# Kernel optimization log

Measured on AMD Instinct MI355X. Metric: run time of the kernel, lower is better.

## Reference

```python
import jax, jax.numpy as jnp
import numpy as np
from jax import lax

# FPN anchor layout: 800x800 image, 3 anchors/loc, strides 4,8,16,32,64
LEVEL_ANCHORS = [120000, 30000, 7500, 1875, 507]
PRE_NMS_TOP_N = 1000   # per level (test mode)
POST_NMS_TOP_N = 1000
NMS_THRESH = 0.7
MIN_SIZE = 1e-3


def setup_inputs() -> dict:
    key = jax.random.key(0)
    k1, k2, k3, k4 = jax.random.split(key, 4)
    A = sum(LEVEL_ANCHORS)
    bs = 2
    predicts = jax.random.normal(k1, (bs, A, 4), jnp.float32) * 0.1
    objectness = jax.random.normal(k2, (bs, A, 1), jnp.float32)
    cxy = jax.random.uniform(k3, (A, 2), jnp.float32, 0.0, 800.0)
    wh = jax.random.uniform(k4, (A, 2), jnp.float32, 16.0, 128.0)
    anchors = jnp.concatenate([cxy - 0.5 * wh, cxy + 0.5 * wh], axis=-1)
    valid_size = jnp.full((bs, 2), 800.0, jnp.float32)  # (w, h) per image
    return {"predicts": predicts, "objectness": objectness,
            "anchors": anchors, "valid_size": valid_size}


def _decode(predicts, anchors):
    # BoxCoder.decoder with weights [1,1,1,1]
    awh = anchors[:, 2:] - anchors[:, :2]          # [A,2]
    axy = anchors[:, :2] + 0.5 * awh               # [A,2]
    xy = axy + predicts[..., :2] * awh             # [bs,A,2] center
    wh = jnp.exp(predicts[..., 2:]) * awh          # [bs,A,2]
    x1y1 = xy - 0.5 * wh
    return jnp.concatenate([x1y1, x1y1 + wh], axis=-1)  # [bs,A,4]


def _per_level_topk_idx(scores):
    # scores: [bs, A] -> concat of per-level top-k indices (global anchor ids)
    idx_list, offset = [], 0
    for n in LEVEL_ANCHORS:
        k = min(PRE_NMS_TOP_N, n)
        _, top = lax.top_k(scores[:, offset:offset + n], k)
        idx_list.append(top + offset)
        offset += n
    return jnp.concatenate(idx_list, axis=1)  # [bs, K]


def _nms_keep(boxes, valid, thresh):
    # boxes sorted by score desc; returns boolean keep mask (sequential NMS)
    x1, y1, x2, y2 = boxes[:, 0], boxes[:, 1], boxes[:, 2], boxes[:, 3]
    area = (x2 - x1) * (y2 - y1)
    xx1 = jnp.maximum(x1[:, None], x1[None, :])
    yy1 = jnp.maximum(y1[:, None], y1[None, :])
    xx2 = jnp.minimum(x2[:, None], x2[None, :])
    yy2 = jnp.minimum(y2[:, None], y2[None, :])
    inter = jnp.maximum(xx2 - xx1, 0.0) * jnp.maximum(yy2 - yy1, 0.0)
    iou = inter / (area[:, None] + area[None, :] - inter + 1e-9)
    sup = iou > thresh                                   # [N,N]
    N = boxes.shape[0]
    ar = jnp.arange(N)

    def body(i, keep):
        suppressed = jnp.any((ar < i) & keep & sup[i])
        return keep.at[i].set(keep[i] & ~suppressed)

    return lax.fori_loop(0, N, body, valid)


def _filter_image(boxes, scores, lvls, wh):
    # boxes [K,4], scores [K], lvls [K] int, wh [2]=(w,h)
    w, h = wh[0], wh[1]
    x1 = jnp.clip(boxes[:, 0], 0.0, w)
    y1 = jnp.clip(boxes[:, 1], 0.0, h)
    x2 = jnp.clip(boxes[:, 2], 0.0, w)
    y2 = jnp.clip(boxes[:, 3], 0.0, h)
    boxes = jnp.stack([x1, y1, x2, y2], axis=-1)
    valid = (x2 - x1 > MIN_SIZE) & (y2 - y1 > MIN_SIZE)
    s = jnp.where(valid, scores, -jnp.inf)
    order = jnp.argsort(-s)
    boxes, s, lvls, valid = boxes[order], s[order], lvls[order], valid[order]
    # batched_nms: offset each level into a disjoint coordinate range
    max_coord = lax.stop_gradient(jnp.max(boxes)) + 1.0
    off = lvls.astype(boxes.dtype) * max_coord
    keep = _nms_keep(lax.stop_gradient(boxes) + off[:, None], valid, NMS_THRESH)
    # take first POST_NMS_TOP_N kept (boxes are score-sorted)
    rank = jnp.cumsum(keep) - 1
    slot = jnp.where(keep & (rank < POST_NMS_TOP_N), rank, POST_NMS_TOP_N)
    out_b = jnp.zeros((POST_NMS_TOP_N + 1, 4), boxes.dtype).at[slot].set(boxes)[:POST_NMS_TOP_N]
    out_s = jnp.zeros((POST_NMS_TOP_N + 1,), s.dtype).at[slot].set(
        jnp.where(keep, s, 0.0))[:POST_NMS_TOP_N]
    return out_b, out_s


def reference(predicts, objectness, anchors, valid_size):
    bs = predicts.shape[0]
    proposals = _decode(predicts, anchors)            # [bs,A,4]
    scores = objectness[..., 0]                       # [bs,A]
    idx = _per_level_topk_idx(scores)                 # [bs,K]
    bidx = jnp.arange(bs)[:, None]
    boxes = proposals[bidx, idx]                      # [bs,K,4]
    sc = scores[bidx, idx]                            # [bs,K]
    levels_all = jnp.concatenate(
        [jnp.full((n,), i, jnp.int32) for i, n in enumerate(LEVEL_ANCHORS)])
    lvl = levels_all[idx]                             # [bs,K]
    final_boxes, final_scores = jax.vmap(_filter_image)(boxes, sc, lvl, valid_size)
    return final_boxes, final_scores
```

## Files before the change

kernel.cpp:

```cpp
#include <hip/hip_runtime.h>

typedef unsigned int u32;
typedef unsigned long long u64;

#define A_TOT    159882
#define BS       2
#define KTOP     1000
#define CAND_CAP 4096
#define HB       4096
#define ABLK     4096
#define NBH      40
#define EPT      16

static const size_t HIST12_OFF   = 0;
static const size_t CUT_OFF      = 131072;
static const size_t CCNT_OFF     = 131104;
static const size_t MAXC_OFF     = 131136;
static const size_t NV_OFF       = 131144;
static const size_t CHUNKANY_OFF = 131200;
static const size_t ZERO_END     = 132480;
static const size_t CAND_OFF     = 132480;
static const size_t LKEY2_OFF    = 394624;
static const size_t LBOX_OFF     = 476544;
static const size_t LSC_OFF      = 640384;
static const size_t RANK_OFF     = 681344;
static const size_t MASK_OFF     = 759168;

__device__ __forceinline__ int level_of(int a) {
  if (a < 120000) return 0;
  if (a < 150000) return 1;
  if (a < 157500) return 2;
  if (a < 159375) return 3;
  return 4;
}

__device__ __forceinline__ u32 dkey(float s) {
  u32 b = __float_as_uint(s);
  return (b & 0x80000000u) ? b : (~b & 0x7FFFFFFFu);
}

__device__ __forceinline__ void decode_clip(const float* __restrict__ pred,
                                            const float* __restrict__ anch,
                                            const float* __restrict__ vs,
                                            int b, int a,
                                            float& x1c, float& y1c, float& x2c, float& y2c,
                                            bool& valid) {
  const float* pp = pred + ((size_t)b * A_TOT + (size_t)a) * 4;
  const float* aa = anch + (size_t)a * 4;
  float ax1 = aa[0], ay1 = aa[1], ax2 = aa[2], ay2 = aa[3];
  float px = pp[0], py = pp[1], pw = pp[2], ph = pp[3];
  float aw  = __fsub_rn(ax2, ax1);
  float ah  = __fsub_rn(ay2, ay1);
  float acx = __fadd_rn(ax1, __fmul_rn(0.5f, aw));
  float acy = __fadd_rn(ay1, __fmul_rn(0.5f, ah));
  float cx  = __fadd_rn(acx, __fmul_rn(px, aw));
  float cy  = __fadd_rn(acy, __fmul_rn(py, ah));
  float w   = __fmul_rn(expf(pw), aw);
  float h   = __fmul_rn(expf(ph), ah);
  float x1  = __fsub_rn(cx, __fmul_rn(0.5f, w));
  float y1  = __fsub_rn(cy, __fmul_rn(0.5f, h));
  float x2  = __fadd_rn(x1, w);
  float y2  = __fadd_rn(y1, h);
  float Wv = vs[b * 2 + 0], Hv = vs[b * 2 + 1];
  x1c = fminf(fmaxf(x1, 0.0f), Wv);
  y1c = fminf(fmaxf(y1, 0.0f), Hv);
  x2c = fminf(fmaxf(x2, 0.0f), Wv);
  y2c = fminf(fmaxf(y2, 0.0f), Hv);
  valid = (__fsub_rn(x2c, x1c) > 0.001f) && (__fsub_rn(y2c, y1c) > 0.001f);
}

__device__ __forceinline__ void bitonic_u64(u64* arr, int N, int t, int nt) {
  for (int k = 2; k <= N; k <<= 1) {
    for (int j = k >> 1; j > 0; j >>= 1) {
      __syncthreads();
      for (int i = t; i < N; i += nt) {
        int ixj = i ^ j;
        if (ixj > i) {
          u64 x = arr[i], y = arr[ixj];
          bool up = ((i & k) == 0);
          if (up ? (x > y) : (x < y)) { arr[i] = y; arr[ixj] = x; }
        }
      }
    }
  }
  __syncthreads();
}

__device__ __forceinline__ u64 shfl_xor_u64(u64 x, int lanemask) {
  u32 lo = (u32)x, hi = (u32)(x >> 32);
  lo = (u32)__shfl_xor((int)lo, lanemask);
  hi = (u32)__shfl_xor((int)hi, lanemask);
  return ((u64)hi << 32) | (u64)lo;
}

__device__ __forceinline__ void regsort2048(u64 v[8], int tid, u64* arr) {
  for (int k = 2; k <= 2048; k <<= 1) {
    for (int j = k >> 1; j > 0; j >>= 1) {
      if (j >= 512) {
        __syncthreads();
#pragma unroll
        for (int e = 0; e < 8; ++e) arr[tid * 8 + e] = v[e];
        __syncthreads();
#pragma unroll
        for (int e = 0; e < 8; ++e) {
          int i = tid * 8 + e, p = i ^ j;
          u64 o = arr[p];
          bool up = ((i & k) == 0);
          bool keepmin = ((i < p) == up);
          v[e] = keepmin ? (v[e] < o ? v[e] : o) : (v[e] > o ? v[e] : o);
        }
      } else if (j >= 8) {
        int dl = j >> 3;
#pragma unroll
        for (int e = 0; e < 8; ++e) {
          int i = tid * 8 + e;
          u64 o = shfl_xor_u64(v[e], dl);
          bool up = ((i & k) == 0);
          bool keepmin = (((tid & dl) == 0) == up);
          v[e] = keepmin ? (v[e] < o ? v[e] : o) : (v[e] > o ? v[e] : o);
        }
      } else {
#pragma unroll
        for (int e = 0; e < 8; ++e) {
          int pe = e ^ j;
          if (pe > e) {
            int i = tid * 8 + e;
            bool up = ((i & k) == 0);
            u64 a = v[e], b2 = v[pe];
            bool sw = up ? (a > b2) : (a < b2);
            if (sw) { v[e] = b2; v[pe] = a; }
          }
        }
      }
    }
  }
  __syncthreads();
#pragma unroll
  for (int e = 0; e < 8; ++e) arr[tid * 8 + e] = v[e];
  __syncthreads();
}

__global__ void k_zero(char* __restrict__ ws) {
  size_t i = (size_t)blockIdx.x * blockDim.x + threadIdx.x;
  if (i * 4 < ZERO_END) ((u32*)ws)[i] = 0u;
}

__global__ void k_hist12(const float* __restrict__ obj, char* __restrict__ ws) {
  __shared__ u32 h[2 * HB];
  int tid = threadIdx.x;
  int b = blockIdx.x / NBH, loc = blockIdx.x % NBH;
  int start = loc * ABLK;
  int l0 = level_of(start);
  if (l0 >= 4) return;
  for (int i = tid; i < 2 * HB; i += 256) h[i] = 0u;
  __syncthreads();
  for (int it = 0; it < EPT; ++it) {
    int a = start + it * 256 + tid;
    if (a < A_TOT) {
      int l = level_of(a);
      if (l < 4) {
        u32 d = dkey(obj[(size_t)b * A_TOT + a]);
        atomicAdd(&h[(u32)(l - l0) * HB + (d >> 20)], 1u);
      }
    }
  }
  __syncthreads();
  int lend = level_of(min(start + ABLK - 1, A_TOT - 1));
  int nseg = ((l0 + 1 <= lend) && (l0 + 1 < 4)) ? 2 : 1;
  for (int s = 0; s < nseg; ++s) {
    u32* gh = (u32*)(ws + HIST12_OFF) + (size_t)(b * 4 + l0 + s) * HB;
    for (int i = tid; i < HB; i += 256) {
      u32 v = h[s * HB + i];
      if (v) atomicAdd(&gh[i], v);
    }
  }
}

__global__ void k_compactsel(const float* __restrict__ obj, char* __restrict__ ws) {
  __shared__ u32 scan[256];
  __shared__ u32 cutv[2];
  __shared__ u32 lcnt[2], gbase[2];
  int tid = threadIdx.x, lane = tid & 63;
  int b = blockIdx.x / NBH, loc = blockIdx.x % NBH;
  int start = loc * ABLK;
  int l0 = level_of(start);
  if (l0 >= 4) return;
  int lend = level_of(min(start + ABLK - 1, A_TOT - 1));
  int nseg = ((l0 + 1 <= lend) && (l0 + 1 < 4)) ? 2 : 1;
  if (tid < 2) lcnt[tid] = 0;
  for (int s = 0; s < nseg; ++s) {
    int seg = b * 4 + l0 + s;
    const u32* gh = (const u32*)(ws + HIST12_OFF) + (size_t)seg * HB;
    u32 vals[16]; u32 acc = 0;
    for (int q = 0; q < 16; ++q) { vals[q] = gh[tid * 16 + q]; acc += vals[q]; }
    __syncthreads();
    scan[tid] = acc; __syncthreads();
    for (int d = 1; d < 256; d <<= 1) {
      u32 x = (tid >= d) ? scan[tid - d] : 0u; __syncthreads();
      scan[tid] += x; __syncthreads();
    }
    u32 incl = scan[tid], prev = incl - acc;
    if (prev < KTOP && incl >= KTOP) {
      u32 run = prev; int cb = HB - 1;
      for (int q = 0; q < 16; ++q) { run += vals[q]; if (run >= KTOP) { cb = tid * 16 + q; break; } }
      cutv[s] = (u32)cb;
      ((u32*)(ws + CUT_OFF))[seg] = (u32)cb;
    }
  }
  __syncthreads();
  u32 dv[EPT], slotv[EPT], passm = 0, sim = 0;
  for (int it = 0; it < EPT; ++it) {
    int a = start + it * 256 + tid;
    bool pass = false; u32 si = 0, d = 0;
    if (a < A_TOT) {
      int l = level_of(a);
      if (l < 4) {
        si = (u32)(l - l0);
        d = dkey(obj[(size_t)b * A_TOT + a]);
        pass = (d >> 20) <= cutv[si];
      }
    }
    dv[it] = d;
    u64 mp = __ballot(pass);
    u64 m1 = __ballot(pass && si == 1);
    u64 m0 = mp & ~m1;
    u32 slot = 0;
    if (m0) {
      int ld = __builtin_ctzll(m0);
      u32 wb = 0;
      if (lane == ld) wb = atomicAdd(&lcnt[0], (u32)__popcll(m0));
      wb = __shfl(wb, ld);
      if (pass && si == 0) slot = wb + (u32)__popcll(m0 & ((1ull << lane) - 1ull));
    }
    if (m1) {
      int ld = __builtin_ctzll(m1);
      u32 wb = 0;
      if (lane == ld) wb = atomicAdd(&lcnt[1], (u32)__popcll(m1));
      wb = __shfl(wb, ld);
      if (pass && si == 1) slot = wb + (u32)__popcll(m1 & ((1ull << lane) - 1ull));
    }
    slotv[it] = slot;
    if (pass) { passm |= 1u << it; if (si) sim |= 1u << it; }
  }
  __syncthreads();
  if (tid < 2)
    gbase[tid] = lcnt[tid] ? atomicAdd((u32*)(ws + CCNT_OFF) + (b * 4 + l0 + tid), lcnt[tid]) : 0u;
  __syncthreads();
  for (int it = 0; it < EPT; ++it) {
    if ((passm >> it) & 1u) {
      int a = start + it * 256 + tid;
      u32 si = (sim >> it) & 1u;
      int seg = b * 4 + l0 + (int)si;
      u32 gslot = gbase[si] + slotv[it];
      if (gslot < CAND_CAP)
        ((u64*)(ws + CAND_OFF))[(size_t)seg * CAND_CAP + gslot] =
            ((u64)dv[it] << 32) | (u32)a;
    }
  }
}

__global__ void k_sortdec(const float* __restrict__ pred, const float* __restrict__ obj,
                          const float* __restrict__ anch, const float* __restrict__ vs,
                          char* __restrict__ ws) {
  __shared__ u64 arr[CAND_CAP];
  __shared__ float4 dboxL[1024];
  __shared__ float dscL[1024];
  __shared__ u64 vmask[16];
  int tid = threadIdx.x, lane = tid & 63, wv = tid >> 6;
  int P = blockIdx.x, b = P / 5, l = P % 5;
  int n;
  if (l == 4) {
    n = 507;
    u64 v[8];
#pragma unroll
    for (int e = 0; e < 8; ++e) {
      int idx = tid * 8 + e;
      if (idx < 507) {
        int a = 159375 + idx;
        v[e] = ((u64)dkey(obj[(size_t)b * A_TOT + a]) << 32) | (u32)a;
      } else v[e] = ~0ull;
    }
    regsort2048(v, tid, arr);
  } else {
    n = KTOP;
    int seg = b * 4 + l;
    u32 cnt = min(((const u32*)(ws + CCNT_OFF))[seg], (u32)CAND_CAP);
    const u64* cand = (const u64*)(ws + CAND_OFF) + (size_t)seg * CAND_CAP;
    if (cnt <= 2048) {
      u64 v[8];
#pragma unroll
      for (int e = 0; e < 8; ++e) {
        int idx = tid * 8 + e;
        v[e] = (idx < (int)cnt) ? cand[idx] : ~0ull;
      }
      regsort2048(v, tid, arr);
    } else {
      for (int i = tid; i < CAND_CAP; i += 256) arr[i] = (i < (int)cnt) ? cand[i] : ~0ull;
      int N = 2048; while (N < (int)cnt) N <<= 1;
      bitonic_u64(arr, N, tid, 256);
    }
  }
  float m = 0.0f;
  for (int k = 0; k < 4; ++k) {
    int j = k * 256 + tid;
    bool vb = false;
    if (j < n) {
      u64 key = arr[j];
      int a = (int)(u32)key;
      float x1, y1, x2, y2; bool valid;
      decode_clip(pred, anch, vs, b, a, x1, y1, x2, y2, valid);
      m = fmaxf(m, fmaxf(fmaxf(x1, y1), fmaxf(x2, y2)));
      dboxL[j] = make_float4(x1, y1, x2, y2);
      dscL[j] = obj[(size_t)b * A_TOT + a];
      vb = valid;
    }
    u64 bal = __ballot(vb);
    if (lane == 0) vmask[k * 4 + wv] = bal;
  }
  for (int off = 32; off; off >>= 1) m = fmaxf(m, __shfl_xor(m, off));
  if (lane == 0) atomicMax((u32*)(ws + MAXC_OFF) + b, __float_as_uint(m));
  __syncthreads();
  if (tid < 64) {
    int base = 0;
    for (int j0 = 0; j0 < n; j0 += 64) {
      int j = j0 + lane;
      bool v = (j < n) && ((vmask[j0 >> 6] >> lane) & 1ull);
      u64 mm = __ballot(v);
      int r = base + __popcll(mm & ((1ull << lane) - 1ull));
      if (v) {
        ((u64*)(ws + LKEY2_OFF))[(size_t)P * 1024 + r] = arr[j];
        ((float4*)(ws + LBOX_OFF))[(size_t)P * 1024 + r] = dboxL[j];
        ((float*)(ws + LSC_OFF))[(size_t)P * 1024 + r] = dscL[j];
      }
      base += __popcll(mm);
    }
    if (lane == 0) ((u32*)(ws + NV_OFF))[P] = (u32)base;
  }
}

__device__ __forceinline__ int lbound(const u64* __restrict__ arr, int n, u64 key) {
  int lo = 0, hi = n;
  while (lo < hi) { int mid = (lo + hi) >> 1; if (arr[mid] < key) lo = mid + 1; else hi = mid; }
  return lo;
}

__global__ void k_maskrank(char* __restrict__ ws) {
  int tid = threadIdx.x, bid = blockIdx.x;
  if (bid < 10) {
    int P = bid, b = P / 5, l = P % 5;
    int nv = (int)((const u32*)(ws + NV_OFF))[P];
    const u64* lkey = (const u64*)(ws + LKEY2_OFF);
    const u32* nvp = (const u32*)(ws + NV_OFF);
    for (int i = tid; i < nv; i += 256) {
      u64 key = lkey[(size_t)P * 1024 + i];
      int r = i;
      for (int l2 = 0; l2 < 5; ++l2) {
        if (l2 == l) continue;
        int P2 = b * 5 + l2;
        r += lbound(lkey + (size_t)P2 * 1024, (int)nvp[P2], key);
      }
      ((u32*)(ws + RANK_OFF))[(size_t)P * 1024 + i] = (u32)r;
    }
  }
  int idx = bid * 256 + tid;
  int w = idx & 15;
  int i = (idx >> 4) & 1023;
  int P = idx >> 14;
  if (P >= 10) return;
  int b = P / 5, l = P % 5;
  int n = (int)((const u32*)(ws + NV_OFF))[P];
  int W = (n + 63) >> 6;
  if (i >= n || w >= W) return;
  float M = __uint_as_float(((const u32*)(ws + MAXC_OFF))[b]);
  float maxc = __fadd_rn(M, 1.0f);
  float off = __fmul_rn((float)l, maxc);
  const float4* lbox = (const float4*)(ws + LBOX_OFF) + (size_t)P * 1024;
  float4 bi = lbox[i];
  bi.x = __fadd_rn(bi.x, off); bi.y = __fadd_rn(bi.y, off);
  bi.z = __fadd_rn(bi.z, off); bi.w = __fadd_rn(bi.w, off);
  float ai = __fmul_rn(__fsub_rn(bi.z, bi.x), __fsub_rn(bi.w, bi.y));
  u64 word = 0;
  int j0 = w << 6;
  int jn = min(64, n - j0);
  for (int jj = 0; jj < jn; ++jj) {
    float4 bj = lbox[j0 + jj];
    bj.x = __fadd_rn(bj.x, off); bj.y = __fadd_rn(bj.y, off);
    bj.z = __fadd_rn(bj.z, off); bj.w = __fadd_rn(bj.w, off);
    float xx1 = fmaxf(bi.x, bj.x);
    float yy1 = fmaxf(bi.y, bj.y);
    float xx2 = fminf(bi.z, bj.z);
    float yy2 = fminf(bi.w, bj.w);
    float iw = fmaxf(__fsub_rn(xx2, xx1), 0.0f);
    float ih = fmaxf(__fsub_rn(yy2, yy1), 0.0f);
    float inter = __fmul_rn(iw, ih);
    float aj = __fmul_rn(__fsub_rn(bj.z, bj.x), __fsub_rn(bj.w, bj.y));
    float den = __fadd_rn(__fsub_rn(__fadd_rn(ai, aj), inter), 1e-9f);
    float iou = __fdiv_rn(inter, den);
    if (iou > 0.7f) word |= (1ull << jj);
  }
  if (i >= j0 && i < j0 + 64) word &= ~(1ull << (i - j0));
  ((u64*)(ws + MASK_OFF))[(size_t)P * 16000 + (size_t)i * W + w] = word;
  if (word)
    atomicOr((u64*)(ws + CHUNKANY_OFF) + (size_t)P * 16 + (i >> 6), 1ull << (i & 63));
}

__global__ __launch_bounds__(320)
void k_scanfin(float* __restrict__ out, char* __restrict__ ws) {
  __shared__ u64 keeps[5][16];
  __shared__ u64 kb[80];
  __shared__ u32 sb[128];
  __shared__ u32 pfx[80];
  __shared__ u32 nvs[5];
  int tid = threadIdx.x, w = tid >> 6, lane = tid & 63;
  int b = blockIdx.x;
  for (int i = tid; i < 80; i += 320) kb[i] = 0ull;
  for (int i = tid; i < 4000; i += 320) out[(size_t)b * 4000 + i] = 0.0f;
  for (int i = tid; i < 1000; i += 320) out[8000 + (size_t)b * 1000 + i] = 0.0f;
  if (tid < 5) nvs[tid] = ((const u32*)(ws + NV_OFF))[b * 5 + tid];

  int P = b * 5 + w;
  int n = (int)((const u32*)(ws + NV_OFF))[P];
  int W = (n + 63) >> 6;
  const u64* maskg = (const u64*)(ws + MASK_OFF) + (size_t)P * 16000;
  u64 ca = (lane < 16) ? ((const u64*)(ws + CHUNKANY_OFF))[(size_t)P * 16 + lane] : 0ull;
  u64 dpre[16];
#pragma unroll
  for (int c = 0; c < 16; ++c) {
    int row = (c << 6) + lane;
    dpre[c] = (c < W && row < n) ? maskg[(size_t)row * W + c] : 0ull;
  }
  u64 removed = 0ull, keepw = 0ull;
#pragma unroll
  for (int c = 0; c < 16; ++c) {
    if (c >= W) break;
    int rb = c << 6;
    int rows = min(64, n - rb);
    u64 rowsmask = (rows == 64) ? ~0ull : ((1ull << rows) - 1ull);
    u64 curw = __shfl(removed, c);
    u64 cand = ~curw & rowsmask;
    u64 ca_c = __shfl(ca, c);
    u64 keptbits;
    u64 anyrows = ca_c & cand;
    if (anyrows == 0ull) {
      keptbits = cand;
    } else {
      u64 diag = dpre[c];
      u64 diagnz = __ballot(diag != 0ull) & cand;
      if (diagnz == 0ull) {
        keptbits = cand;
      } else {
        u64 remw = curw | ~rowsmask;
        u64 kept = 0ull;
        int pos = 0;
        u64 work = diagnz;
        while (work) {
          int s = __builtin_ctzll(work); work &= work - 1;
          u64 range = (1ull << s) - (1ull << pos);
          kept |= ~remw & range;
          bool k = ((remw >> s) & 1ull) == 0ull;
          u64 dr = __shfl(diag, s);
          if (k) { kept |= 1ull << s; remw |= dr; }
          pos = s + 1;
        }
        u64 tail = (pos >= 64) ? 0ull : (~0ull << pos);
        kept |= ~remw & tail & rowsmask;
        keptbits = kept;
      }
      u64 todo = keptbits & ca_c;
      while (todo) {
        int r0 = __builtin_ctzll(todo); todo &= todo - 1;
        int r1 = -1, r2 = -1, r3 = -1;
        if (todo) { r1 = __builtin_ctzll(todo); todo &= todo - 1; }
        if (todo) { r2 = __builtin_ctzll(todo); todo &= todo - 1; }
        if (todo) { r3 = __builtin_ctzll(todo); todo &= todo - 1; }
        u64 v0 = 0, v1 = 0, v2 = 0, v3 = 0;
        if (lane < W) {
          v0 = maskg[(size_t)(rb + r0) * W + lane];
          if (r1 >= 0) v1 = maskg[(size_t)(rb + r1) * W + lane];
          if (r2 >= 0) v2 = maskg[(size_t)(rb + r2) * W + lane];
          if (r3 >= 0) v3 = maskg[(size_t)(rb + r3) * W + lane];
        }
        removed |= v0 | v1 | v2 | v3;
      }
    }
    if (lane == c) keepw |= keptbits;
  }
  if (lane < 16) keeps[w][lane] = keepw;
  __syncthreads();

  const u32* rank = (const u32*)(ws + RANK_OFF);
  for (int idx = tid; idx < 5120; idx += 320) {
    int p = idx >> 10, i = idx & 1023;
    if (i < (int)nvs[p] && ((keeps[p][i >> 6] >> (i & 63)) & 1ull)) {
      u32 r = rank[(size_t)(b * 5 + p) * 1024 + i];
      atomicOr(&kb[r >> 6], 1ull << (r & 63));
    }
  }
  __syncthreads();
  if (tid < 128) sb[tid] = (tid < 80) ? (u32)__popcll(kb[tid]) : 0u;
  __syncthreads();
  for (int d = 1; d < 128; d <<= 1) {
    u32 x = (tid < 128 && tid >= d) ? sb[tid - d] : 0u;
    __syncthreads();
    if (tid < 128) sb[tid] += x;
    __syncthreads();
  }
  if (tid < 80) pfx[tid] = sb[tid] - (u32)__popcll(kb[tid]);
  __syncthreads();
  for (int idx = tid; idx < 5120; idx += 320) {
    int p = idx >> 10, i = idx & 1023;
    if (i < (int)nvs[p] && ((keeps[p][i >> 6] >> (i & 63)) & 1ull)) {
      int Pp = b * 5 + p;
      u32 r = rank[(size_t)Pp * 1024 + i];
      u64 word = kb[r >> 6];
      int slot = (int)pfx[r >> 6] + __popcll(word & ((1ull << (r & 63)) - 1ull));
      if (slot < KTOP) {
        float4 bx = ((const float4*)(ws + LBOX_OFF))[(size_t)Pp * 1024 + i];
        float s = ((const float*)(ws + LSC_OFF))[(size_t)Pp * 1024 + i];
        float* ob = out + ((size_t)b * KTOP + slot) * 4;
        ob[0] = bx.x; ob[1] = bx.y; ob[2] = bx.z; ob[3] = bx.w;
        out[8000 + (size_t)b * KTOP + slot] = s;
      }
    }
  }
}

extern "C" void kernel_launch(void* const* d_in, const int* in_sizes, int n_in,
                              void* d_out, int out_size, void* d_ws, size_t ws_size,
                              hipStream_t stream) {
  const float* pred = (const float*)d_in[0];
  const float* obj  = (const float*)d_in[1];
  const float* anch = (const float*)d_in[2];
  const float* vs   = (const float*)d_in[3];
  float* out = (float*)d_out;
  char* ws = (char*)d_ws;
  (void)in_sizes; (void)n_in; (void)out_size; (void)ws_size;

  int gZ = (int)((ZERO_END / 4 + 255) / 256);
  k_zero      <<<gZ,        256, 0, stream>>>(ws);
  k_hist12    <<<BS * NBH,  256, 0, stream>>>(obj, ws);
  k_compactsel<<<BS * NBH,  256, 0, stream>>>(obj, ws);
  k_sortdec   <<<10,        256, 0, stream>>>(pred, obj, anch, vs, ws);
  k_maskrank  <<<640,       256, 0, stream>>>(ws);
  k_scanfin   <<<2,         320, 0, stream>>>(out, ws);
}
```

Before: 193.8 us.

## Widen sort-decode kernel to 1024 threads and decode boxes before the sort

The per-level sort-and-decode kernel now runs with 1024 threads, each holding two keys instead of eight. Cross-wave bitonic stages ping-pong between two shared buffers, so each stage needs one barrier instead of two. Box decode and clipping now happen before the sort, indexed by candidate slot. To support this, the candidate key packs the anchor id and the slot into its low bits, and the compaction step becomes a single-pass ballot across 16 waves. The aim is to spread this kernel's serial sort and decode over more threads. The risk is that later kernels reading the stored keys must accept the new low-bit encoding.

```diff
diff --git a/kernel.cpp b/kernel.cpp
--- a/kernel.cpp
+++ b/kernel.cpp
@@ -37,6 +37,10 @@
 __device__ __forceinline__ u32 dkey(float s) {
   u32 b = __float_as_uint(s);
   return (b & 0x80000000u) ? b : (~b & 0x7FFFFFFFu);
+}
+__device__ __forceinline__ float dkey_inv(u32 d) {
+  u32 b = (d & 0x80000000u) ? d : (~d & 0x7FFFFFFFu);
+  return __uint_as_float(b);
 }
 
 __device__ __forceinline__ void decode_clip(const float* __restrict__ pred,
@@ -93,51 +97,45 @@
   return ((u64)hi << 32) | (u64)lo;
 }
 
-__device__ __forceinline__ void regsort2048(u64 v[8], int tid, u64* arr) {
+__device__ __forceinline__ u64* regsort2048x(u64 v[2], int tid, u64* bufA, u64* bufB) {
+  u64* bufs[2] = {bufA, bufB};
+  int cur = 0;
   for (int k = 2; k <= 2048; k <<= 1) {
     for (int j = k >> 1; j > 0; j >>= 1) {
-      if (j >= 512) {
+      if (j == 1) {
+        bool up = (((2 * tid) & k) == 0);
+        u64 a = v[0], b2 = v[1];
+        bool sw = up ? (a > b2) : (a < b2);
+        if (sw) { v[0] = b2; v[1] = a; }
+      } else if (j <= 64) {
+        int dl = j >> 1;
+        bool up = (((2 * tid) & k) == 0);
+        bool low = ((tid & dl) == 0);
+        bool keepmin = (low == up);
+#pragma unroll
+        for (int e = 0; e < 2; ++e) {
+          u64 o = shfl_xor_u64(v[e], dl);
+          v[e] = keepmin ? (v[e] < o ? v[e] : o) : (v[e] > o ? v[e] : o);
+        }
+      } else {
+        u64* B = bufs[cur]; cur ^= 1;
+        B[2 * tid] = v[0]; B[2 * tid + 1] = v[1];
         __syncthreads();
 #pragma unroll
-        for (int e = 0; e < 8; ++e) arr[tid * 8 + e] = v[e];
-        __syncthreads();
-#pragma unroll
-        for (int e = 0; e < 8; ++e) {
-          int i = tid * 8 + e, p = i ^ j;
-          u64 o = arr[p];
+        for (int e = 0; e < 2; ++e) {
+          int i = 2 * tid + e, p = i ^ j;
+          u64 o = B[p];
           bool up = ((i & k) == 0);
           bool keepmin = ((i < p) == up);
           v[e] = keepmin ? (v[e] < o ? v[e] : o) : (v[e] > o ? v[e] : o);
         }
-      } else if (j >= 8) {
-        int dl = j >> 3;
-#pragma unroll
-        for (int e = 0; e < 8; ++e) {
-          int i = tid * 8 + e;
-          u64 o = shfl_xor_u64(v[e], dl);
-          bool up = ((i & k) == 0);
-          bool keepmin = (((tid & dl) == 0) == up);
-          v[e] = keepmin ? (v[e] < o ? v[e] : o) : (v[e] > o ? v[e] : o);
-        }
-      } else {
-#pragma unroll
-        for (int e = 0; e < 8; ++e) {
-          int pe = e ^ j;
-          if (pe > e) {
-            int i = tid * 8 + e;
-            bool up = ((i & k) == 0);
-            u64 a = v[e], b2 = v[pe];
-            bool sw = up ? (a > b2) : (a < b2);
-            if (sw) { v[e] = b2; v[pe] = a; }
-          }
-        }
-      }
-    }
-  }
-  __syncthreads();
-#pragma unroll
-  for (int e = 0; e < 8; ++e) arr[tid * 8 + e] = v[e];
-  __syncthreads();
+      }
+    }
+  }
+  u64* B = bufs[cur];
+  B[2 * tid] = v[0]; B[2 * tid + 1] = v[1];
+  __syncthreads();
+  return B;
 }
 
 __global__ void k_zero(char* __restrict__ ws) {
@@ -254,87 +252,111 @@
       u32 gslot = gbase[si] + slotv[it];
       if (gslot < CAND_CAP)
         ((u64*)(ws + CAND_OFF))[(size_t)seg * CAND_CAP + gslot] =
-            ((u64)dv[it] << 32) | (u32)a;
-    }
-  }
-}
-
-__global__ void k_sortdec(const float* __restrict__ pred, const float* __restrict__ obj,
-                          const float* __restrict__ anch, const float* __restrict__ vs,
-                          char* __restrict__ ws) {
-  __shared__ u64 arr[CAND_CAP];
-  __shared__ float4 dboxL[1024];
-  __shared__ float dscL[1024];
-  __shared__ u64 vmask[16];
+            ((u64)dv[it] << 32) | ((u64)(u32)a << 12) | (u64)gslot;
+    }
+  }
+}
+
+__global__ __launch_bounds__(1024)
+void k_sortdec(const float* __restrict__ pred, const float* __restrict__ obj,
+               const float* __restrict__ anch, const float* __restrict__ vs,
+               char* __restrict__ ws) {
+  __shared__ u64 bufAB[4096];
+  __shared__ float4 dboxS[2048];
+  __shared__ float dscS[2048];
+  __shared__ u32 validS[2048];
+  __shared__ u64 cm[16];
+  u64* bufA = bufAB; u64* bufB = bufAB + 2048;
   int tid = threadIdx.x, lane = tid & 63, wv = tid >> 6;
   int P = blockIdx.x, b = P / 5, l = P % 5;
   int n;
+  u64* S;
   if (l == 4) {
     n = 507;
-    u64 v[8];
+    u64 v[2];
 #pragma unroll
-    for (int e = 0; e < 8; ++e) {
-      int idx = tid * 8 + e;
+    for (int e = 0; e < 2; ++e) {
+      int idx = 2 * tid + e;
       if (idx < 507) {
         int a = 159375 + idx;
-        v[e] = ((u64)dkey(obj[(size_t)b * A_TOT + a]) << 32) | (u32)a;
+        float sc = obj[(size_t)b * A_TOT + a];
+        float x1, y1, x2, y2; bool valid;
+        decode_clip(pred, anch, vs, b, a, x1, y1, x2, y2, valid);
+        dboxS[idx] = make_float4(x1, y1, x2, y2);
+        dscS[idx] = sc;
+        validS[idx] = valid ? 1u : 0u;
+        v[e] = ((u64)dkey(sc) << 32) | ((u64)(u32)a << 12) | (u64)idx;
       } else v[e] = ~0ull;
     }
-    regsort2048(v, tid, arr);
+    S = regsort2048x(v, tid, bufA, bufB);
   } else {
     n = KTOP;
     int seg = b * 4 + l;
     u32 cnt = min(((const u32*)(ws + CCNT_OFF))[seg], (u32)CAND_CAP);
     const u64* cand = (const u64*)(ws + CAND_OFF) + (size_t)seg * CAND_CAP;
     if (cnt <= 2048) {
-      u64 v[8];
+      u64 v[2];
 #pragma unroll
-      for (int e = 0; e < 8; ++e) {
-        int idx = tid * 8 + e;
-        v[e] = (idx < (int)cnt) ? cand[idx] : ~0ull;
-      }
-      regsort2048(v, tid, arr);
+      for (int e = 0; e < 2; ++e) {
+        int idx = 2 * tid + e;
+        if (idx < (int)cnt) {
+          u64 key = cand[idx];
+          int a = (int)((key >> 12) & 0x3FFFFu);
+          float x1, y1, x2, y2; bool valid;
+          decode_clip(pred, anch, vs, b, a, x1, y1, x2, y2, valid);
+          dboxS[idx] = make_float4(x1, y1, x2, y2);
+          dscS[idx] = dkey_inv((u32)(key >> 32));
+          validS[idx] = valid ? 1u : 0u;
+          v[e] = key;
+        } else v[e] = ~0ull;
+      }
+      S = regsort2048x(v, tid, bufA, bufB);
     } else {
-      for (int i = tid; i < CAND_CAP; i += 256) arr[i] = (i < (int)cnt) ? cand[i] : ~0ull;
       int N = 2048; while (N < (int)cnt) N <<= 1;
-      bitonic_u64(arr, N, tid, 256);
+      for (int i = tid; i < N; i += 1024) bufAB[i] = (i < (int)cnt) ? cand[i] : ~0ull;
+      bitonic_u64(bufAB, N, tid, 1024);
+      for (int j = tid; j < KTOP; j += 1024) {
+        u64 key = bufAB[j];
+        int a = (int)((key >> 12) & 0x3FFFFu);
+        float x1, y1, x2, y2; bool valid;
+        decode_clip(pred, anch, vs, b, a, x1, y1, x2, y2, valid);
+        dboxS[j] = make_float4(x1, y1, x2, y2);
+        dscS[j] = dkey_inv((u32)(key >> 32));
+        validS[j] = valid ? 1u : 0u;
+        bufAB[j] = (key & ~0xFFFull) | (u64)j;
+      }
+      __syncthreads();
+      S = bufAB;
     }
   }
   float m = 0.0f;
-  for (int k = 0; k < 4; ++k) {
-    int j = k * 256 + tid;
-    bool vb = false;
-    if (j < n) {
-      u64 key = arr[j];
-      int a = (int)(u32)key;
-      float x1, y1, x2, y2; bool valid;
-      decode_clip(pred, anch, vs, b, a, x1, y1, x2, y2, valid);
-      m = fmaxf(m, fmaxf(fmaxf(x1, y1), fmaxf(x2, y2)));
-      dboxL[j] = make_float4(x1, y1, x2, y2);
-      dscL[j] = obj[(size_t)b * A_TOT + a];
-      vb = valid;
-    }
-    u64 bal = __ballot(vb);
-    if (lane == 0) vmask[k * 4 + wv] = bal;
+  for (int j = tid; j < n; j += 1024) {
+    int slot = (int)(S[j] & 0xFFFull);
+    float4 bx = dboxS[slot];
+    m = fmaxf(m, fmaxf(fmaxf(bx.x, bx.y), fmaxf(bx.z, bx.w)));
   }
   for (int off = 32; off; off >>= 1) m = fmaxf(m, __shfl_xor(m, off));
   if (lane == 0) atomicMax((u32*)(ws + MAXC_OFF) + b, __float_as_uint(m));
-  __syncthreads();
-  if (tid < 64) {
+  {
+    int j = wv * 64 + lane;
+    bool val = (j < n) && (validS[(int)(S[j] & 0xFFFull)] != 0u);
+    u64 mask = __ballot(val);
+    if (lane == 0) cm[wv] = mask;
+    __syncthreads();
     int base = 0;
-    for (int j0 = 0; j0 < n; j0 += 64) {
-      int j = j0 + lane;
-      bool v = (j < n) && ((vmask[j0 >> 6] >> lane) & 1ull);
-      u64 mm = __ballot(v);
-      int r = base + __popcll(mm & ((1ull << lane) - 1ull));
-      if (v) {
-        ((u64*)(ws + LKEY2_OFF))[(size_t)P * 1024 + r] = arr[j];
-        ((float4*)(ws + LBOX_OFF))[(size_t)P * 1024 + r] = dboxL[j];
-        ((float*)(ws + LSC_OFF))[(size_t)P * 1024 + r] = dscL[j];
-      }
-      base += __popcll(mm);
-    }
-    if (lane == 0) ((u32*)(ws + NV_OFF))[P] = (u32)base;
+    for (int w2 = 0; w2 < wv; ++w2) base += __popcll(cm[w2]);
+    if (val) {
+      int r = base + __popcll(mask & ((1ull << lane) - 1ull));
+      int slot = (int)(S[j] & 0xFFFull);
+      ((u64*)(ws + LKEY2_OFF))[(size_t)P * 1024 + r] = S[j];
+      ((float4*)(ws + LBOX_OFF))[(size_t)P * 1024 + r] = dboxS[slot];
+      ((float*)(ws + LSC_OFF))[(size_t)P * 1024 + r] = dscS[slot];
+    }
+    if (tid == 0) {
+      int tot = 0;
+      for (int w2 = 0; w2 < 16; ++w2) tot += __popcll(cm[w2]);
+      ((u32*)(ws + NV_OFF))[P] = (u32)tot;
+    }
   }
 }
 
@@ -540,7 +562,7 @@
   k_zero      <<<gZ,        256, 0, stream>>>(ws);
   k_hist12    <<<BS * NBH,  256, 0, stream>>>(obj, ws);
   k_compactsel<<<BS * NBH,  256, 0, stream>>>(obj, ws);
-  k_sortdec   <<<10,        256, 0, stream>>>(pred, obj, anch, vs, ws);
+  k_sortdec   <<<10,       1024, 0, stream>>>(pred, obj, anch, vs, ws);
   k_maskrank  <<<640,       256, 0, stream>>>(ws);
   k_scanfin   <<<2,         320, 0, stream>>>(out, ws);
 }
```

Result: faster. 173.3 us (-10.6%).
